# Kernel optimization log

Hardware: AMD Instinct MI355X
Metric: run time of the kernel (lower is better)

## Reference

```python
import jax, jax.numpy as jnp
import numpy as np

B, N, D = 8, 2048, 256
SCALE = 10.0  # self.scale_constant

def setup_inputs() -> dict:
    key = jax.random.key(0)
    ks = jax.random.split(key, 8)
    x = jax.random.normal(ks[0], (B, N, D), dtype=jnp.float32)
    recycler_mask = jax.random.randint(ks[1], (N, N), 0, 2, dtype=jnp.int32)
    s = 1.0 / np.sqrt(D)
    Wq = jax.random.uniform(ks[2], (D, D), jnp.float32, -s, s)
    bq = jax.random.uniform(ks[3], (D,), jnp.float32, -s, s)
    Wk = jax.random.uniform(ks[4], (D, D), jnp.float32, -s, s)
    bk = jax.random.uniform(ks[5], (D,), jnp.float32, -s, s)
    Wl = jax.random.uniform(ks[6], (1, D), jnp.float32, -s, s)
    bl = jax.random.uniform(ks[7], (1,), jnp.float32, -s, s)
    return {"x": x, "recycler_mask": recycler_mask, "Wq": Wq, "bq": bq,
            "Wk": Wk, "bk": bk, "Wl": Wl, "bl": bl}

def reference(x, recycler_mask, Wq, bq, Wk, bk, Wl, bl):
    # query/key linear projections (torch Linear: x @ W.T + b)
    query = jnp.einsum('bnd,ed->bne', x, Wq) + bq  # (B,N,D)
    key_ = jnp.einsum('bnd,ed->bne', x, Wk) + bk   # (B,N,D)
    scores = jnp.einsum('bnd,bmd->bnm', query, key_)  # (B,N,N)
    scores = SCALE * jnp.tanh(scores)
    scores = jnp.where(recycler_mask[None, :, :] == 0, -jnp.inf, scores)
    picked_logit = jnp.einsum('bnd,ed->bne', x, Wl) + bl  # (B,N,1)
    return picked_logit, scores
```

## Files before the change

### kernel.cpp

```cpp
#include <hip/hip_runtime.h>
#include <math.h>

#define B_ 8
#define N_ 2048
#define D_ 256
#define SCALE_ 10.0f
#define NEG_SENTINEL_ (-1.0e30f)

#define BM 128
#define BN 128
#define BK 64
#define KTILES (D_ / BK)
#define TILE_ELEMS (BM * BK)

typedef unsigned short ushort_t;
typedef __attribute__((ext_vector_type(8))) short bf16x8;
typedef __attribute__((ext_vector_type(4))) float f32x4;

__device__ __forceinline__ ushort_t f2bf(float f) {
    union { float f; unsigned int u; } a; a.f = f;
    unsigned int r = a.u + 0x7fffu + ((a.u >> 16) & 1u);
    return (ushort_t)(r >> 16);
}

__device__ __forceinline__ void gl16(const void* g, void* l) {
    __builtin_amdgcn_global_load_lds(
        (const __attribute__((address_space(1))) unsigned int*)g,
        (__attribute__((address_space(3))) unsigned int*)l, 16, 0, 0);
}


__global__ __launch_bounds__(256) void rcy_proj_v6(
    const float* __restrict__ x,
    const float* __restrict__ Wq, const float* __restrict__ bq,
    const float* __restrict__ Wk, const float* __restrict__ bk,
    const float* __restrict__ Wl, const float* __restrict__ bl,
    ushort_t* __restrict__ Qo, ushort_t* __restrict__ Ko,
    float* __restrict__ logit)
{
    __shared__ ushort_t As[BM * BK];
    __shared__ ushort_t Bqs[BN * BK];
    __shared__ ushort_t Bks[BN * BK];

    const int m0 = blockIdx.x * BM;
    const int n0 = blockIdx.y * BN;
    const int t  = threadIdx.x;
    const int w  = t >> 6, l = t & 63;
    const int wr = w >> 1, wc = w & 1;
    const int srow0 = t >> 3;
    const int schunk = t & 7;
    const bool do_logit = (blockIdx.y == 0);

    f32x4 accq[4][4] = {};
    f32x4 acck[4][4] = {};
    float lacc[4] = {0.f, 0.f, 0.f, 0.f};

    for (int k0 = 0; k0 < D_; k0 += BK) {
        __syncthreads();
        float4 wl0, wl1;
        if (do_logit) {
            const float4* wlp = (const float4*)(Wl + k0 + schunk * 8);
            wl0 = wlp[0]; wl1 = wlp[1];
        }
        #pragma unroll
        for (int p = 0; p < 4; ++p) {
            const int row = p * 32 + srow0;
            const int off = ((row * 128 + schunk * 16) ^ ((row & 7) << 4));
            const float4* xa = (const float4*)(x + (size_t)(m0 + row) * D_ + k0 + schunk * 8);
            float4 f0 = xa[0], f1 = xa[1];
            union { bf16x8 v; ushort_t u[8]; } pa;
            pa.u[0]=f2bf(f0.x); pa.u[1]=f2bf(f0.y); pa.u[2]=f2bf(f0.z); pa.u[3]=f2bf(f0.w);
            pa.u[4]=f2bf(f1.x); pa.u[5]=f2bf(f1.y); pa.u[6]=f2bf(f1.z); pa.u[7]=f2bf(f1.w);
            *(bf16x8*)((char*)As + off) = pa.v;
            if (do_logit) {
                lacc[p] += f0.x*wl0.x + f0.y*wl0.y + f0.z*wl0.z + f0.w*wl0.w
                         + f1.x*wl1.x + f1.y*wl1.y + f1.z*wl1.z + f1.w*wl1.w;
            }
            const float4* qa = (const float4*)(Wq + (size_t)(n0 + row) * D_ + k0 + schunk * 8);
            float4 g0 = qa[0], g1 = qa[1];
            union { bf16x8 v; ushort_t u[8]; } pb;
            pb.u[0]=f2bf(g0.x); pb.u[1]=f2bf(g0.y); pb.u[2]=f2bf(g0.z); pb.u[3]=f2bf(g0.w);
            pb.u[4]=f2bf(g1.x); pb.u[5]=f2bf(g1.y); pb.u[6]=f2bf(g1.z); pb.u[7]=f2bf(g1.w);
            *(bf16x8*)((char*)Bqs + off) = pb.v;
            const float4* ka = (const float4*)(Wk + (size_t)(n0 + row) * D_ + k0 + schunk * 8);
            float4 h0 = ka[0], h1 = ka[1];
            union { bf16x8 v; ushort_t u[8]; } pc;
            pc.u[0]=f2bf(h0.x); pc.u[1]=f2bf(h0.y); pc.u[2]=f2bf(h0.z); pc.u[3]=f2bf(h0.w);
            pc.u[4]=f2bf(h1.x); pc.u[5]=f2bf(h1.y); pc.u[6]=f2bf(h1.z); pc.u[7]=f2bf(h1.w);
            *(bf16x8*)((char*)Bks + off) = pc.v;
        }
        __syncthreads();
        #pragma unroll
        for (int ks = 0; ks < 2; ++ks) {
            bf16x8 af[4], bqf[4], bkf[4];
            #pragma unroll
            for (int f = 0; f < 4; ++f) {
                const int m = wr * 64 + f * 16 + (l & 15);
                const int aoff = ((m * 128 + ks * 64 + (l >> 4) * 16) ^ ((m & 7) << 4));
                af[f] = *(const bf16x8*)((const char*)As + aoff);
                const int n = wc * 64 + f * 16 + (l & 15);
                const int boff = ((n * 128 + ks * 64 + (l >> 4) * 16) ^ ((n & 7) << 4));
                bqf[f] = *(const bf16x8*)((const char*)Bqs + boff);
                bkf[f] = *(const bf16x8*)((const char*)Bks + boff);
            }
            #pragma unroll
            for (int i = 0; i < 4; ++i)
                #pragma unroll
                for (int j = 0; j < 4; ++j) {
                    accq[i][j] = __builtin_amdgcn_mfma_f32_16x16x32_bf16(af[i], bqf[j], accq[i][j], 0, 0, 0);
                    acck[i][j] = __builtin_amdgcn_mfma_f32_16x16x32_bf16(af[i], bkf[j], acck[i][j], 0, 0, 0);
                }
        }
    }

    const int b  = m0 >> 11;
    const int rb = (m0 & 2047) >> 7;
    const size_t tbase = (((size_t)b * 16 + rb) * KTILES + (blockIdx.y * 2 + wc)) * (size_t)TILE_ELEMS;
    #pragma unroll
    for (int j = 0; j < 4; ++j) {
        const int col = n0 + wc * 64 + j * 16 + (l & 15);
        const float bvq = bq[col];
        const float bvk = bk[col];
        const int cl = j * 16 + (l & 15);
        #pragma unroll
        for (int i = 0; i < 4; ++i) {
            #pragma unroll
            for (int r = 0; r < 4; ++r) {
                const int rl = wr * 64 + i * 16 + (l >> 4) * 4 + r;
                const int sidx = (rl * BK + cl) ^ ((rl & 7) << 3);
                Qo[tbase + (size_t)sidx] = f2bf(accq[i][j][r] + bvq);
                Ko[tbase + (size_t)sidx] = f2bf(acck[i][j][r] + bvk);
            }
        }
    }

    if (do_logit) {
        const float bl0 = bl[0];
        #pragma unroll
        for (int p = 0; p < 4; ++p) {
            float s = lacc[p];
            s += __shfl_down(s, 4);
            s += __shfl_down(s, 2);
            s += __shfl_down(s, 1);
            if (schunk == 0) logit[m0 + p * 32 + srow0] = s + bl0;
        }
    }
}

__global__ __launch_bounds__(256) void rcy_scores_v8(
    const ushort_t* __restrict__ Qt, const ushort_t* __restrict__ Kt,
    const int* __restrict__ mask, float* __restrict__ out)
{
    __shared__ ushort_t lds[2][2][TILE_ELEMS];

    const int bx = blockIdx.x;
    const int by = blockIdx.y;
    const int bz = blockIdx.z;
    const int t  = threadIdx.x;
    const int w  = t >> 6, l = t & 63;
    const int wr = w >> 1, wc = w & 1;

    const char* gA = (const char*)(Qt + (((size_t)bz * 16 + bx) * KTILES) * TILE_ELEMS);
    const char* gB = (const char*)(Kt + (((size_t)bz * 16 + by) * KTILES) * TILE_ELEMS);

    f32x4 acc[4][4] = {};

    #define STAGE(buf, kb) { \
        const char* sa = gA + (size_t)(kb) * (TILE_ELEMS * 2); \
        const char* sb = gB + (size_t)(kb) * (TILE_ELEMS * 2); \
        char* la = (char*)&lds[buf][0][0]; \
        char* lb = (char*)&lds[buf][1][0]; \
        _Pragma("unroll") \
        for (int q = 0; q < 4; ++q) { \
            gl16(sa + q * 4096 + t * 16, la + q * 4096 + t * 16); \
            gl16(sb + q * 4096 + t * 16, lb + q * 4096 + t * 16); \
        } }

    #define COMPUTE(buf) { \
        const char* As_ = (const char*)&lds[buf][0][0]; \
        const char* Bs_ = (const char*)&lds[buf][1][0]; \
        _Pragma("unroll") \
        for (int ks = 0; ks < 2; ++ks) { \
            bf16x8 af[4], bf[4]; \
            _Pragma("unroll") \
            for (int f = 0; f < 4; ++f) { \
                const int m = wr * 64 + f * 16 + (l & 15); \
                const int aoff = (m * 128 + ks * 64 + (l >> 4) * 16) ^ ((m & 7) << 4); \
                af[f] = *(const bf16x8*)(As_ + aoff); \
                const int n = wc * 64 + f * 16 + (l & 15); \
                const int boff = (n * 128 + ks * 64 + (l >> 4) * 16) ^ ((n & 7) << 4); \
                bf[f] = *(const bf16x8*)(Bs_ + boff); \
            } \
            _Pragma("unroll") \
            for (int i = 0; i < 4; ++i) \
                _Pragma("unroll") \
                for (int j = 0; j < 4; ++j) \
                    acc[i][j] = __builtin_amdgcn_mfma_f32_16x16x32_bf16(af[i], bf[j], acc[i][j], 0, 0, 0); \
        } }

    STAGE(0, 0);
    STAGE(1, 1);
    asm volatile("s_waitcnt vmcnt(8)" ::: "memory");
    __builtin_amdgcn_s_barrier();
    COMPUTE(0);
    __builtin_amdgcn_s_barrier();
    STAGE(0, 2);
    asm volatile("s_waitcnt vmcnt(8)" ::: "memory");
    __builtin_amdgcn_s_barrier();
    COMPUTE(1);
    __builtin_amdgcn_s_barrier();
    STAGE(1, 3);
    asm volatile("s_waitcnt vmcnt(8)" ::: "memory");
    __builtin_amdgcn_s_barrier();
    COMPUTE(0);
    __builtin_amdgcn_s_barrier();
    asm volatile("s_waitcnt vmcnt(0)" ::: "memory");
    __builtin_amdgcn_s_barrier();
    COMPUTE(1);

    const int bm0 = bx * BM, bn0 = by * BN;
    float* outb = out + (size_t)bz * N_ * N_;
    #pragma unroll
    for (int i = 0; i < 4; ++i) {
        #pragma unroll
        for (int r = 0; r < 4; ++r) {
            const int row = bm0 + wr * 64 + i * 16 + (l >> 4) * 4 + r;
            #pragma unroll
            for (int j = 0; j < 4; ++j) {
                const int col = bn0 + wc * 64 + j * 16 + (l & 15);
                const int mk = mask[(size_t)row * N_ + col];
                const float v = acc[i][j][r];
                const float e = __expf(v + v);
                const float s = fmaf(-20.0f, __builtin_amdgcn_rcpf(e + 1.0f), SCALE_);
                outb[(size_t)row * N_ + col] = mk ? s : NEG_SENTINEL_;
            }
        }
    }
    #undef STAGE
    #undef COMPUTE
}

extern "C" void kernel_launch(void* const* d_in, const int* in_sizes, int n_in,
                              void* d_out, int out_size, void* d_ws, size_t ws_size,
                              hipStream_t stream)
{
    const float* x  = (const float*)d_in[0];
    const int* mask = (const int*)d_in[1];
    const float* Wq = (const float*)d_in[2];
    const float* bq = (const float*)d_in[3];
    const float* Wk = (const float*)d_in[4];
    const float* bk = (const float*)d_in[5];
    const float* Wl = (const float*)d_in[6];
    const float* bl = (const float*)d_in[7];

    float* logit  = (float*)d_out;
    float* scores = (float*)d_out + (size_t)B_ * N_;

    ushort_t* Qw = (ushort_t*)d_ws;
    ushort_t* Kw = Qw + (size_t)B_ * 16 * KTILES * TILE_ELEMS;

    rcy_proj_v6<<<dim3((B_*N_)/BM, D_/BN), 256, 0, stream>>>(
        x, Wq, bq, Wk, bk, Wl, bl, Qw, Kw, logit);
    rcy_scores_v8<<<dim3(N_/BM, N_/BN, B_), 256, 0, stream>>>(Qw, Kw, mask, scores);
}
```

Before: 69.17 us.

## Pack mask into bitfield once and swizzle scores tile order for locality

Adds a pre-pass kernel that packs the int32 mask into 64-bit ballot words, so the scores kernel reads one bit per element instead of a 4-byte int. It is repeated per batch, cutting mask traffic from 16 MB times 8 reads to a small bitmap. Also remaps the grid to a 1D index with 4x4 tile grouping for better Q/K cache reuse. Costs an extra kernel launch and an LDS staging step with a barrier.

```diff
diff --git a/kernel.cpp b/kernel.cpp
--- a/kernel.cpp
+++ b/kernel.cpp
@@ -14,6 +14,7 @@
 #define TILE_ELEMS (BM * BK)
 
 typedef unsigned short ushort_t;
+typedef unsigned long long u64_t;
 typedef __attribute__((ext_vector_type(8))) short bf16x8;
 typedef __attribute__((ext_vector_type(4))) float f32x4;
 
@@ -147,21 +148,36 @@
     }
 }
 
-__global__ __launch_bounds__(256) void rcy_scores_v8(
+__global__ __launch_bounds__(256) void rcy_maskpack(
+    const int* __restrict__ mask, u64_t* __restrict__ bits)
+{
+    const int gid = blockIdx.x * 256 + threadIdx.x;
+    const u64_t bal = __ballot(mask[gid] != 0);
+    if ((threadIdx.x & 63) == 0) bits[gid >> 6] = bal;
+}
+
+__global__ __launch_bounds__(256) void rcy_scores_v9(
     const ushort_t* __restrict__ Qt, const ushort_t* __restrict__ Kt,
-    const int* __restrict__ mask, float* __restrict__ out)
+    const u64_t* __restrict__ bits, float* __restrict__ out)
 {
     __shared__ ushort_t lds[2][2][TILE_ELEMS];
-
-    const int bx = blockIdx.x;
-    const int by = blockIdx.y;
-    const int bz = blockIdx.z;
+    __shared__ u64_t bitlds[256];
+
+    const int g  = blockIdx.x;
+    const int bz = g >> 8;
+    const int r_ = g & 255;
+    const int grp = r_ >> 4;
+    const int within = r_ & 15;
+    const int bx = (grp & 3) * 4 + (within & 3);
+    const int by = (grp >> 2) * 4 + (within >> 2);
     const int t  = threadIdx.x;
     const int w  = t >> 6, l = t & 63;
     const int wr = w >> 1, wc = w & 1;
 
     const char* gA = (const char*)(Qt + (((size_t)bz * 16 + bx) * KTILES) * TILE_ELEMS);
     const char* gB = (const char*)(Kt + (((size_t)bz * 16 + by) * KTILES) * TILE_ELEMS);
+
+    const u64_t mybits = bits[(size_t)(bx * BM + (t >> 1)) * (N_ / 64) + by * 2 + (t & 1)];
 
     f32x4 acc[4][4] = {};
 
@@ -217,6 +233,8 @@
     asm volatile("s_waitcnt vmcnt(0)" ::: "memory");
     __builtin_amdgcn_s_barrier();
     COMPUTE(1);
+    bitlds[t] = mybits;
+    __syncthreads();
 
     const int bm0 = bx * BM, bn0 = by * BN;
     float* outb = out + (size_t)bz * N_ * N_;
@@ -224,11 +242,13 @@
     for (int i = 0; i < 4; ++i) {
         #pragma unroll
         for (int r = 0; r < 4; ++r) {
-            const int row = bm0 + wr * 64 + i * 16 + (l >> 4) * 4 + r;
+            const int rl = wr * 64 + i * 16 + (l >> 4) * 4 + r;
+            const u64_t mrow = bitlds[rl * 2 + wc];
+            const int row = bm0 + rl;
             #pragma unroll
             for (int j = 0; j < 4; ++j) {
                 const int col = bn0 + wc * 64 + j * 16 + (l & 15);
-                const int mk = mask[(size_t)row * N_ + col];
+                const int mk = (int)((mrow >> (j * 16 + (l & 15))) & 1ull);
                 const float v = acc[i][j][r];
                 const float e = __expf(v + v);
                 const float s = fmaf(-20.0f, __builtin_amdgcn_rcpf(e + 1.0f), SCALE_);
@@ -258,8 +278,10 @@
 
     ushort_t* Qw = (ushort_t*)d_ws;
     ushort_t* Kw = Qw + (size_t)B_ * 16 * KTILES * TILE_ELEMS;
-
+    u64_t* bits  = (u64_t*)(Kw + (size_t)B_ * 16 * KTILES * TILE_ELEMS);
+
+    rcy_maskpack<<<dim3((N_*N_)/256), 256, 0, stream>>>(mask, bits);
     rcy_proj_v6<<<dim3((B_*N_)/BM, D_/BN), 256, 0, stream>>>(
         x, Wq, bq, Wk, bk, Wl, bl, Qw, Kw, logit);
-    rcy_scores_v8<<<dim3(N_/BM, N_/BN, B_), 256, 0, stream>>>(Qw, Kw, mask, scores);
-}
+    rcy_scores_v9<<<dim3((N_/BM) * (N_/BN) * B_), 256, 0, stream>>>(Qw, Kw, bits, scores);
+}
```

Result: no change. 68.25 us (-1.3%).
